# Optimization experiments

Measured on AMD Instinct MI355X. Metric: run time of the kernel, lower is better.

The kernel has to match this reference:

```python
import jax, jax.numpy as jnp
import numpy as np

# data_shape = (w, h, d, t); x viewed as torch (N, 1, D=w, H=h, W=d)
W_, H_, D_, T_ = 128, 128, 64, 100
INP = W_ * H_ * D_
K = 1


def _lin(n):
    # align_corners=False normalized coords (PyTorch affine_grid default)
    return (2.0 * jnp.arange(n, dtype=jnp.float32) + 1.0) / n - 1.0


def affine_grid(theta, Dm, Hm, Wm):
    # theta: (N, 3, 4) -> grid: (N, D, H, W, 3) with grid[...,0]=x(W), 1=y(H), 2=z(D)
    xs, ys, zs = _lin(Wm), _lin(Hm), _lin(Dm)
    base = jnp.stack([
        jnp.broadcast_to(xs[None, None, :], (Dm, Hm, Wm)),
        jnp.broadcast_to(ys[None, :, None], (Dm, Hm, Wm)),
        jnp.broadcast_to(zs[:, None, None], (Dm, Hm, Wm)),
        jnp.ones((Dm, Hm, Wm), jnp.float32),
    ], axis=-1)  # (D,H,W,4)
    return jnp.einsum('dhwb,nab->ndhwa', base, theta)


def grid_sample_3d(vol, grid):
    # vol: (N,D,H,W); grid: (N,D,H,W,3); trilinear, zeros padding, align_corners=False
    N, D, H, Wd = vol.shape
    ix = ((grid[..., 0] + 1.0) * Wd - 1.0) * 0.5
    iy = ((grid[..., 1] + 1.0) * H - 1.0) * 0.5
    iz = ((grid[..., 2] + 1.0) * D - 1.0) * 0.5
    x0 = jnp.floor(ix); y0 = jnp.floor(iy); z0 = jnp.floor(iz)
    tx, ty, tz = ix - x0, iy - y0, iz - z0
    x0i, y0i, z0i = x0.astype(jnp.int32), y0.astype(jnp.int32), z0.astype(jnp.int32)
    b = jnp.arange(N)[:, None, None, None]
    out = jnp.zeros_like(ix)
    for dz in (0, 1):
        for dy in (0, 1):
            for dx in (0, 1):
                xc, yc, zc = x0i + dx, y0i + dy, z0i + dz
                w = ((tx if dx else 1.0 - tx) * (ty if dy else 1.0 - ty)
                     * (tz if dz else 1.0 - tz))
                valid = ((xc >= 0) & (xc < Wd) & (yc >= 0) & (yc < H)
                         & (zc >= 0) & (zc < D))
                v = vol[b,
                        jnp.clip(zc, 0, D - 1),
                        jnp.clip(yc, 0, H - 1),
                        jnp.clip(xc, 0, Wd - 1)]
                out = out + jnp.where(valid, w * v, 0.0)
    return out


def setup_inputs() -> dict:
    key = jax.random.key(0)
    k1, k2, k3, k4 = jax.random.split(key, 4)
    x = jax.random.normal(k1, (8, INP), dtype=jnp.float32)
    r_index = jax.random.randint(k2, (8,), 0, T_)
    ident = jnp.array([[1., 0., 0., 0.], [0., 1., 0., 0.], [0., 0., 1., 0.]],
                      dtype=jnp.float32)
    theta = (jnp.tile(ident[None], (T_, 1, 1))
             + 0.01 * jax.random.normal(k3, (T_, 3, 4), dtype=jnp.float32))
    ln_weight = jax.random.normal(k4, (K, INP), dtype=jnp.float32) / np.sqrt(INP)
    return {"x": x, "r_index": r_index, "theta": theta, "ln_weight": ln_weight}


def reference(x, r_index, theta, ln_weight):
    n = x.shape[0]
    th = theta[r_index]                      # (n,3,4)
    vol = x.reshape(n, W_, H_, D_)           # torch (n,1,D=w,H=h,W=d), channel squeezed
    grid = affine_grid(th, W_, H_, D_)       # (n,w,h,d,3)
    x_reg = grid_sample_3d(vol, grid).reshape(n, INP)
    L = (x_reg @ ln_weight.T) @ ln_weight    # rank-k bottleneck: ln(x) @ ln.weight
    return x_reg, L
```

## Files before the change

kernel.cpp:

```cpp
#include <hip/hip_runtime.h>

#define INP (128*128*64)
#define NB 8
#define NBLK2 2048

typedef __attribute__((ext_vector_type(4))) float f32x4;
typedef __attribute__((ext_vector_type(2))) float f32x2;
typedef int v4i __attribute__((ext_vector_type(4)));

#if __has_builtin(__builtin_amdgcn_make_buffer_rsrc) && __has_builtin(__builtin_amdgcn_raw_buffer_load_b32)
#define RSRC_T __amdgpu_buffer_rsrc_t
__device__ __forceinline__ RSRC_T make_rsrc(const float* p) {
    return __builtin_amdgcn_make_buffer_rsrc((void*)p, (short)0, INP * 4, 0x00020000);
}
__device__ __forceinline__ float bload(RSRC_T r, int boff) {
    return __builtin_bit_cast(float, __builtin_amdgcn_raw_buffer_load_b32(r, boff, 0, 0));
}
#else
#define RSRC_T v4i
__device__ __forceinline__ RSRC_T make_rsrc(const float* p) {
    union { const float* p; unsigned u[2]; } pun; pun.p = p;
    RSRC_T r;
    r.x = (int)pun.u[0]; r.y = (int)pun.u[1]; r.z = INP * 4; r.w = 0x00020000;
    return r;
}
__device__ __forceinline__ float bload(RSRC_T r, int boff) {
    return __builtin_amdgcn_raw_buffer_load_f32(r, boff, 0, 0);
}
#endif

#if __has_builtin(__builtin_amdgcn_raw_buffer_load_b64)
__device__ __forceinline__ f32x2 bload2(RSRC_T r, int boff) {
    return __builtin_bit_cast(f32x2, __builtin_amdgcn_raw_buffer_load_b64(r, boff, 0, 0));
}
#else
__device__ __forceinline__ f32x2 bload2(RSRC_T r, int boff) {
    f32x2 v; v.x = bload(r, boff); v.y = bload(r, boff + 4); return v;
}
#endif

__device__ __forceinline__ float wave_reduce(float v) {
    #pragma unroll
    for (int off = 32; off > 0; off >>= 1) v += __shfl_down(v, off, 64);
    return v;
}

struct Prep {
    int o[4];
    float wa, wb, wy0, wy1, wz0, wz1;
};

__device__ __forceinline__ Prep prep_s(float ix, float iy, float iz) {
    const float fx = floorf(ix), fy = floorf(iy), fz = floorf(iz);
    const int x0 = (int)fx, y0 = (int)fy, z0 = (int)fz;
    const int x1 = x0 + 1,  y1 = y0 + 1,  z1 = z0 + 1;

    const float wx1 = ix - fx, wx0 = 1.f - wx1;
    Prep p;
    p.wy1 = iy - fy; p.wy0 = 1.f - p.wy1;
    p.wz1 = iz - fz; p.wz0 = 1.f - p.wz1;
    p.wy0 = ((unsigned)y0 < 128u) ? p.wy0 : 0.f;
    p.wy1 = ((unsigned)y1 < 128u) ? p.wy1 : 0.f;
    p.wz0 = ((unsigned)z0 < 128u) ? p.wz0 : 0.f;
    p.wz1 = ((unsigned)z1 < 128u) ? p.wz1 : 0.f;

    const float wx0z = ((unsigned)x0 < 64u) ? wx0 : 0.f;
    const float wx1z = ((unsigned)x1 < 64u) ? wx1 : 0.f;
    const bool hi = (x0 >= 63);
    const bool lo = (x0 < 0);
    p.wa = lo ? wx1z : (hi ? 0.f : wx0z);
    p.wb = hi ? wx0z : (lo ? 0.f : wx1z);

    const int yc0 = min(max(y0, 0), 127), yc1 = min(max(y1, 0), 127);
    const int zc0 = min(max(z0, 0), 127), zc1 = min(max(z1, 0), 127);
    const int xpb = min(max(x0, 0), 62) << 2;
    const int yb0 = (yc0 << 8) + xpb, yb1 = (yc1 << 8) + xpb;
    const int zb0 = zc0 << 15,        zb1 = zc1 << 15;
    p.o[0] = zb0 + yb0; p.o[1] = zb0 + yb1;
    p.o[2] = zb1 + yb0; p.o[3] = zb1 + yb1;
    return p;
}

__device__ __forceinline__ float blend_s(const Prep& p, const f32x2 v[4]) {
    const float bx00 = fmaf(p.wb, v[0].y, p.wa * v[0].x);
    const float bx01 = fmaf(p.wb, v[1].y, p.wa * v[1].x);
    const float bx10 = fmaf(p.wb, v[2].y, p.wa * v[2].x);
    const float bx11 = fmaf(p.wb, v[3].y, p.wa * v[3].x);
    const float by0  = fmaf(p.wy1, bx01, p.wy0 * bx00);
    const float by1  = fmaf(p.wy1, bx11, p.wy0 * bx10);
    return fmaf(p.wz1, by1, p.wz0 * by0);
}

__global__ __launch_bounds__(256) void k_sample(
    const float* __restrict__ x, const int* __restrict__ r_index,
    const float* __restrict__ theta, const float* __restrict__ lnw,
    float* __restrict__ x_reg, float* __restrict__ partial)
{
    const int b  = blockIdx.y;
    const int i2 = blockIdx.x * 256 + threadIdx.x;
    const int w0 = (i2 & 31) << 1;
    const int h  = (i2 >> 5) & 127;
    const int d  = i2 >> 12;

    const f32x2 w2 = ((const f32x2*)lnw)[i2];

    const float xs = fmaf((float)w0, 1.f/32.f, 1.f/64.f  - 1.f);
    const float ys = fmaf((float)h,  1.f/64.f, 1.f/128.f - 1.f);
    const float zs = fmaf((float)d,  1.f/64.f, 1.f/128.f - 1.f);

    const float* __restrict__ t = theta + r_index[b] * 12;
    const float gx = fmaf(t[0], xs, fmaf(t[1], ys, fmaf(t[2],  zs, t[3])));
    const float gy = fmaf(t[4], xs, fmaf(t[5], ys, fmaf(t[6],  zs, t[7])));
    const float gz = fmaf(t[8], xs, fmaf(t[9], ys, fmaf(t[10], zs, t[11])));
    const float ix0 = fmaf(gx, 32.f, 31.5f);
    const float iy0 = fmaf(gy, 64.f, 63.5f);
    const float iz0 = fmaf(gz, 64.f, 63.5f);

    const RSRC_T r = make_rsrc(x + (size_t)b * INP);

    const Prep p0 = prep_s(ix0, iy0, iz0);
    const Prep p1 = prep_s(ix0 + t[0], iy0 + 2.f*t[4], iz0 + 2.f*t[8]);

    f32x2 v0[4], v1[4];
    #pragma unroll
    for (int j = 0; j < 4; ++j) v0[j] = bload2(r, p0.o[j]);
    #pragma unroll
    for (int j = 0; j < 4; ++j) v1[j] = bload2(r, p1.o[j]);

    const float o0 = blend_s(p0, v0);
    const float o1 = blend_s(p1, v1);

    f32x2 o; o.x = o0; o.y = o1;
    __builtin_nontemporal_store(o, (f32x2*)(x_reg + (size_t)b * INP) + i2);

    float acc = fmaf(o1, w2.y, o0 * w2.x);
    acc = wave_reduce(acc);
    __shared__ float sm[4];
    if ((threadIdx.x & 63) == 0) sm[threadIdx.x >> 6] = acc;
    __syncthreads();
    if (threadIdx.x == 0)
        partial[b * NBLK2 + blockIdx.x] = sm[0] + sm[1] + sm[2] + sm[3];
}

__global__ __launch_bounds__(256) void k_outer(
    const float* __restrict__ lnw, const float* __restrict__ partial,
    float* __restrict__ L)
{
    const int b   = blockIdx.y;
    const int tid = threadIdx.x;

    const f32x4* p4 = (const f32x4*)(partial + b * NBLK2);
    const f32x4 a0 = p4[tid];
    const f32x4 a1 = p4[tid + 256];
    float v = (a0.x + a0.y) + (a0.z + a0.w) + (a1.x + a1.y) + (a1.z + a1.w);
    v = wave_reduce(v);
    __shared__ float sm[4];
    __shared__ float smt;
    if ((tid & 63) == 0) sm[tid >> 6] = v;
    __syncthreads();
    if (tid == 0) smt = (sm[0] + sm[1]) + (sm[2] + sm[3]);
    __syncthreads();
    const float sb = smt;

    const int base = blockIdx.x * 2048 + tid;
    const f32x4* w4p = (const f32x4*)lnw;
    f32x4* L4 = (f32x4*)L + (size_t)b * (INP / 4);
    #pragma unroll
    for (int k = 0; k < 8; ++k) {
        const f32x4 w4 = w4p[base + k * 256];
        __builtin_nontemporal_store(sb * w4, L4 + base + k * 256);
    }
}

extern "C" void kernel_launch(void* const* d_in, const int* in_sizes, int n_in,
                              void* d_out, int out_size, void* d_ws, size_t ws_size,
                              hipStream_t stream) {
    const float* x       = (const float*)d_in[0];
    const int*   r_index = (const int*)d_in[1];
    const float* theta   = (const float*)d_in[2];
    const float* lnw     = (const float*)d_in[3];

    float* x_reg = (float*)d_out;
    float* L     = (float*)d_out + (size_t)NB * INP;

    float* partial = (float*)d_ws;

    dim3 grid1(NBLK2, NB);
    k_sample<<<grid1, 256, 0, stream>>>(x, r_index, theta, lnw, x_reg, partial);
    dim3 grid2(128, NB);
    k_outer<<<grid2, 256, 0, stream>>>(lnw, partial, L);
}
```

Measured before the change: 33.96 us.

## Stage per-block source slab in LDS for trilinear gathers

Each block works out the z/y extent of the voxels its threads sample, using wave and block min/max reductions. When that extent fits in a 4x16x64 slab, it loads the slab with 128-bit buffer loads into shared memory and runs the 8-tap gathers from LDS. Otherwise it falls back to the original global gather path. The aim is to replace scattered global 64-bit gathers with coalesced loads, at the cost of extra barriers, reductions and LDS use per block.

```diff
diff --git a/kernel.cpp b/kernel.cpp
--- a/kernel.cpp
+++ b/kernel.cpp
@@ -3,9 +3,12 @@
 #define INP (128*128*64)
 #define NB 8
 #define NBLK2 2048
+#define ZCAP 4
+#define YCAP 16
 
 typedef __attribute__((ext_vector_type(4))) float f32x4;
 typedef __attribute__((ext_vector_type(2))) float f32x2;
+typedef __attribute__((ext_vector_type(4))) unsigned int u32x4;
 typedef int v4i __attribute__((ext_vector_type(4)));
 
 #if __has_builtin(__builtin_amdgcn_make_buffer_rsrc) && __has_builtin(__builtin_amdgcn_raw_buffer_load_b32)
@@ -39,9 +42,30 @@
 }
 #endif
 
+#if __has_builtin(__builtin_amdgcn_raw_buffer_load_b128)
+__device__ __forceinline__ f32x4 bload4(RSRC_T r, int boff) {
+    return __builtin_bit_cast(f32x4, __builtin_amdgcn_raw_buffer_load_b128(r, boff, 0, 0));
+}
+#else
+__device__ __forceinline__ f32x4 bload4(RSRC_T r, int boff) {
+    f32x2 a = bload2(r, boff), b = bload2(r, boff + 8);
+    f32x4 v; v.x = a.x; v.y = a.y; v.z = b.x; v.w = b.y; return v;
+}
+#endif
+
 __device__ __forceinline__ float wave_reduce(float v) {
     #pragma unroll
     for (int off = 32; off > 0; off >>= 1) v += __shfl_down(v, off, 64);
+    return v;
+}
+__device__ __forceinline__ int wave_rmin(int v) {
+    #pragma unroll
+    for (int off = 32; off > 0; off >>= 1) v = min(v, __shfl_down(v, off, 64));
+    return v;
+}
+__device__ __forceinline__ int wave_rmax(int v) {
+    #pragma unroll
+    for (int off = 32; off > 0; off >>= 1) v = max(v, __shfl_down(v, off, 64));
     return v;
 }
 
@@ -91,16 +115,60 @@
     return fmaf(p.wz1, by1, p.wz0 * by0);
 }
 
+__device__ __forceinline__ float sample_lds(const float* __restrict__ slab,
+                                            float ix, float iy, float iz,
+                                            int zorg, int yorg) {
+    const float fx = floorf(ix), fy = floorf(iy), fz = floorf(iz);
+    const int x0 = (int)fx, y0 = (int)fy, z0 = (int)fz;
+
+    const float wx1 = ix - fx, wx0 = 1.f - wx1;
+    float wy1 = iy - fy, wy0 = 1.f - wy1;
+    float wz1 = iz - fz, wz0 = 1.f - wz1;
+    wy0 = ((unsigned)y0       < 128u) ? wy0 : 0.f;
+    wy1 = ((unsigned)(y0 + 1) < 128u) ? wy1 : 0.f;
+    wz0 = ((unsigned)z0       < 128u) ? wz0 : 0.f;
+    wz1 = ((unsigned)(z0 + 1) < 128u) ? wz1 : 0.f;
+
+    const float wx0z = ((unsigned)x0 < 64u) ? wx0 : 0.f;
+    const float wx1z = ((unsigned)(x0 + 1) < 64u) ? wx1 : 0.f;
+    const bool hi = (x0 >= 63);
+    const bool lo = (x0 < 0);
+    const float wa = lo ? wx1z : (hi ? 0.f : wx0z);
+    const float wb = hi ? wx0z : (lo ? 0.f : wx1z);
+
+    const int xp = min(max(x0, 0), 62);
+    const int base = ((z0 - zorg) << 10) + ((y0 - yorg) << 6) + xp;
+
+    const float v000 = slab[base],        v001 = slab[base + 1];
+    const float v010 = slab[base + 64],   v011 = slab[base + 65];
+    const float v100 = slab[base + 1024], v101 = slab[base + 1025];
+    const float v110 = slab[base + 1088], v111 = slab[base + 1089];
+
+    const float bx00 = fmaf(wb, v001, wa * v000);
+    const float bx01 = fmaf(wb, v011, wa * v010);
+    const float bx10 = fmaf(wb, v101, wa * v100);
+    const float bx11 = fmaf(wb, v111, wa * v110);
+    const float by0  = fmaf(wy1, bx01, wy0 * bx00);
+    const float by1  = fmaf(wy1, bx11, wy0 * bx10);
+    return fmaf(wz1, by1, wz0 * by0);
+}
+
 __global__ __launch_bounds__(256) void k_sample(
     const float* __restrict__ x, const int* __restrict__ r_index,
     const float* __restrict__ theta, const float* __restrict__ lnw,
     float* __restrict__ x_reg, float* __restrict__ partial)
 {
-    const int b  = blockIdx.y;
-    const int i2 = blockIdx.x * 256 + threadIdx.x;
-    const int w0 = (i2 & 31) << 1;
-    const int h  = (i2 >> 5) & 127;
-    const int d  = i2 >> 12;
+    __shared__ float slab[ZCAP * YCAP * 64];
+    __shared__ int   red[4][4];
+    __shared__ int   bnd[3];
+    __shared__ float smt[4];
+
+    const int b   = blockIdx.y;
+    const int tid = threadIdx.x;
+    const int i2  = blockIdx.x * 256 + tid;
+    const int w0  = (i2 & 31) << 1;
+    const int h   = (i2 >> 5) & 127;
+    const int d   = i2 >> 12;
 
     const f32x2 w2 = ((const f32x2*)lnw)[i2];
 
@@ -115,31 +183,70 @@
     const float ix0 = fmaf(gx, 32.f, 31.5f);
     const float iy0 = fmaf(gy, 64.f, 63.5f);
     const float iz0 = fmaf(gz, 64.f, 63.5f);
+    const float ix1 = ix0 + t[0];
+    const float iy1 = iy0 + 2.f * t[4];
+    const float iz1 = iz0 + 2.f * t[8];
+
+    const int y00 = (int)floorf(iy0), z00 = (int)floorf(iz0);
+    const int y10 = (int)floorf(iy1), z10 = (int)floorf(iz1);
+    int mnz = wave_rmin(min(z00, z10));
+    int mxz = wave_rmax(max(z00, z10));
+    int mny = wave_rmin(min(y00, y10));
+    int mxy = wave_rmax(max(y00, y10));
+    if ((tid & 63) == 0) {
+        red[tid >> 6][0] = mnz; red[tid >> 6][1] = mxz;
+        red[tid >> 6][2] = mny; red[tid >> 6][3] = mxy;
+    }
+    __syncthreads();
+    if (tid == 0) {
+        int a0 = min(min(red[0][0], red[1][0]), min(red[2][0], red[3][0]));
+        int a1 = max(max(red[0][1], red[1][1]), max(red[2][1], red[3][1]));
+        int a2 = min(min(red[0][2], red[1][2]), min(red[2][2], red[3][2]));
+        int a3 = max(max(red[0][3], red[1][3]), max(red[2][3], red[3][3]));
+        bnd[0] = a0; bnd[1] = a2;
+        bnd[2] = ((a1 - a0 + 2) <= ZCAP) & ((a3 - a2 + 2) <= YCAP);
+    }
+    __syncthreads();
+    const int zorg = bnd[0], yorg = bnd[1], ok = bnd[2];
 
     const RSRC_T r = make_rsrc(x + (size_t)b * INP);
-
-    const Prep p0 = prep_s(ix0, iy0, iz0);
-    const Prep p1 = prep_s(ix0 + t[0], iy0 + 2.f*t[4], iz0 + 2.f*t[8]);
-
-    f32x2 v0[4], v1[4];
-    #pragma unroll
-    for (int j = 0; j < 4; ++j) v0[j] = bload2(r, p0.o[j]);
-    #pragma unroll
-    for (int j = 0; j < 4; ++j) v1[j] = bload2(r, p1.o[j]);
-
-    const float o0 = blend_s(p0, v0);
-    const float o1 = blend_s(p1, v1);
+    float o0, o1;
+
+    if (ok) {
+        const int row = tid >> 2, part = tid & 3;
+        const int gzr = min(max(zorg + (row >> 4), 0), 127);
+        const int gyr = min(max(yorg + (row & 15), 0), 127);
+        const int src = (gzr << 15) + (gyr << 8) + (part << 6);
+        float* dst = slab + (row << 6) + (part << 4);
+        #pragma unroll
+        for (int k = 0; k < 4; ++k) {
+            const f32x4 v = bload4(r, src + k * 16);
+            *(f32x4*)(dst + k * 4) = v;
+        }
+        __syncthreads();
+        o0 = sample_lds(slab, ix0, iy0, iz0, zorg, yorg);
+        o1 = sample_lds(slab, ix1, iy1, iz1, zorg, yorg);
+    } else {
+        const Prep p0 = prep_s(ix0, iy0, iz0);
+        const Prep p1 = prep_s(ix1, iy1, iz1);
+        f32x2 v0[4], v1[4];
+        #pragma unroll
+        for (int j = 0; j < 4; ++j) v0[j] = bload2(r, p0.o[j]);
+        #pragma unroll
+        for (int j = 0; j < 4; ++j) v1[j] = bload2(r, p1.o[j]);
+        o0 = blend_s(p0, v0);
+        o1 = blend_s(p1, v1);
+    }
 
     f32x2 o; o.x = o0; o.y = o1;
     __builtin_nontemporal_store(o, (f32x2*)(x_reg + (size_t)b * INP) + i2);
 
     float acc = fmaf(o1, w2.y, o0 * w2.x);
     acc = wave_reduce(acc);
-    __shared__ float sm[4];
-    if ((threadIdx.x & 63) == 0) sm[threadIdx.x >> 6] = acc;
-    __syncthreads();
-    if (threadIdx.x == 0)
-        partial[b * NBLK2 + blockIdx.x] = sm[0] + sm[1] + sm[2] + sm[3];
+    if ((tid & 63) == 0) smt[tid >> 6] = acc;
+    __syncthreads();
+    if (tid == 0)
+        partial[b * NBLK2 + blockIdx.x] = smt[0] + smt[1] + smt[2] + smt[3];
 }
 
 __global__ __launch_bounds__(256) void k_outer(
```

Result: slower. 59.36 us (+74.8%).
